# Kernel optimization log

Hardware: AMD Instinct MI355X
Metric: run time of the kernel (lower is better)

The kernel has to match this reference:

```python
import jax, jax.numpy as jnp
import numpy as np

B, N, IN_DIM, OUT_DIM, H = 4, 4096, 128, 128, 4
D = OUT_DIM // H  # head_dim = 32
NEG_SLOPE = 0.2


def setup_inputs() -> dict:
    key = jax.random.key(0)
    k_h, k_w = jax.random.split(key)
    h = jax.random.normal(k_h, (B, N, IN_DIM), dtype=jnp.float32)
    W = jax.random.normal(k_w, (OUT_DIM, IN_DIM), dtype=jnp.float32) * (1.0 / np.sqrt(IN_DIM))
    return {"h": h, "W": W}


def reference(h, W):
    b, n, _ = h.shape
    # Linear projection (no bias), split heads: [b, n, H, D]
    Wh = jnp.einsum('bni,oi->bno', h, W).reshape(b, n, H, D)
    # Per-head dense scores e = Wh @ Wh^T: [b, H, n, n]
    e = jnp.einsum('bnhd,bmhd->bhnm', Wh, Wh)
    # LeakyReLU-modified scores, row softmax (dropout = identity in eval)
    attn = jax.nn.softmax(jax.nn.leaky_relu(e, NEG_SLOPE), axis=-1)
    # Weighted aggregation: [b, n, H, D] -> [b, n, OUT_DIM]
    h_prime = jnp.einsum('bhnm,bmhd->bnhd', attn, Wh).reshape(b, n, H * D)
    return h_prime
```

## Files before the change

kernel.cpp:

```cpp
#include <hip/hip_runtime.h>

typedef __attribute__((ext_vector_type(8))) _Float16 f16x8;
typedef __attribute__((ext_vector_type(2))) __fp16 fp16x2;
typedef __attribute__((ext_vector_type(4))) float f32x4;
typedef __attribute__((ext_vector_type(4))) int i32x4;

#define NB 4
#define NN 4096
#define NH 4
#define ND 32
#define NEG_SL 0.2f
#define BQ 64
#define BK 128
#define KSTR 80
#define VSTR 272
#define CSC 1.2011224f
#define THR 10.0f

static __device__ __forceinline__ ushort f32_to_f16u(float f) {
  union { _Float16 h; ushort u; } c;
  c.h = (_Float16)f;
  return c.u;
}
static __device__ __forceinline__ float f16u_to_f32(ushort u) {
  union { _Float16 h; ushort u; } c;
  c.u = u;
  return (float)c.h;
}
static __device__ __forceinline__ unsigned cvt_pk_f16(float a, float b) {
  union { fp16x2 h; unsigned u; } c;
  c.h = __builtin_amdgcn_cvt_pkrtz(a, b);
  return c.u;
}
template <int CTRL>
static __device__ __forceinline__ float row_ror(float x) {
  return __int_as_float(__builtin_amdgcn_update_dpp(
      __float_as_int(x), __float_as_int(x), CTRL, 0xf, 0xf, true));
}
static __device__ __forceinline__ float rmax16(float v) {
  v = fmaxf(v, row_ror<0x121>(v));
  v = fmaxf(v, row_ror<0x122>(v));
  v = fmaxf(v, row_ror<0x124>(v));
  v = fmaxf(v, row_ror<0x128>(v));
  return v;
}
static __device__ __forceinline__ float rsum16(float v) {
  v += row_ror<0x121>(v);
  v += row_ror<0x122>(v);
  v += row_ror<0x124>(v);
  v += row_ror<0x128>(v);
  return v;
}

__global__ __launch_bounds__(256) void proj_kernel(const float* __restrict__ hm,
                                                   const float* __restrict__ Wm,
                                                   ushort* __restrict__ whh,
                                                   ushort* __restrict__ whl) {
  __shared__ float sWT[128 * 128];
  __shared__ float sH[64][128];

  const int t = threadIdx.x;
  const long rowbase = (long)blockIdx.x * 64;

  for (int i = t; i < 4096; i += 256) {
    const int o = i & 127, k4 = i >> 7;
    const float4 w = *(const float4*)(Wm + o * 128 + k4 * 4);
    sWT[(k4 * 4 + 0) * 128 + o] = w.x;
    sWT[(k4 * 4 + 1) * 128 + o] = w.y;
    sWT[(k4 * 4 + 2) * 128 + o] = w.z;
    sWT[(k4 * 4 + 3) * 128 + o] = w.w;
  }
  for (int i = t; i < 64 * 128 / 4; i += 256) {
    *((float4*)(&sH[0][0]) + i) = *((const float4*)(hm + rowbase * 128) + i);
  }
  __syncthreads();

  const int oc = (t & 31) * 4;
  const int nr = (t >> 5) * 8;

  float acc[8][4];
#pragma unroll
  for (int r = 0; r < 8; ++r)
#pragma unroll
    for (int j = 0; j < 4; ++j) acc[r][j] = 0.f;

  for (int k = 0; k < 128; ++k) {
    const float4 wv = *(const float4*)(&sWT[k * 128 + oc]);
#pragma unroll
    for (int r = 0; r < 8; ++r) {
      const float hv = sH[nr + r][k];
      acc[r][0] = fmaf(hv, wv.x, acc[r][0]);
      acc[r][1] = fmaf(hv, wv.y, acc[r][1]);
      acc[r][2] = fmaf(hv, wv.z, acc[r][2]);
      acc[r][3] = fmaf(hv, wv.w, acc[r][3]);
    }
  }

  const int hh = oc >> 5;
  const int d0 = oc & 31;
#pragma unroll
  for (int r = 0; r < 8; ++r) {
    const long gn = rowbase + nr + r;
    const long b = gn >> 12;
    const long n = gn & 4095;
    unsigned hi_[4], lo_[4];
#pragma unroll
    for (int j = 0; j < 4; ++j) {
      const float v = acc[r][j] * CSC;
      const ushort h16 = f32_to_f16u(v);
      hi_[j] = h16;
      lo_[j] = f32_to_f16u(v - f16u_to_f32(h16));
    }
    const size_t idx = (((size_t)(b * NH + hh)) * NN + n) * ND + d0;
    uint2 ph, pl;
    ph.x = hi_[0] | (hi_[1] << 16);
    ph.y = hi_[2] | (hi_[3] << 16);
    pl.x = lo_[0] | (lo_[1] << 16);
    pl.y = lo_[2] | (lo_[3] << 16);
    *(uint2*)(whh + idx) = ph;
    *(uint2*)(whl + idx) = pl;
  }
}

__global__ __launch_bounds__(256, 3) void attn_kernel(const ushort* __restrict__ whh,
                                                      const ushort* __restrict__ whl,
                                                      float* __restrict__ out) {
  __shared__ __align__(16) char sK[BK * KSTR];
  __shared__ __align__(16) char sVt[32 * VSTR];
  __shared__ __align__(16) char sP[4][6144];

  const int t = threadIdx.x;
  const int wid = t >> 6;
  const int lane = t & 63;
  const int qr = lane & 15;
  const int kg = lane >> 4;

  int bid = blockIdx.x;
  bid = (bid & 7) * 128 + (bid >> 3);
  const int qt = bid & 63;
  const int bh = bid >> 6;
  const ushort* __restrict__ baseh = whh + (size_t)bh * NN * ND;
  const ushort* __restrict__ basel = whl + (size_t)bh * NN * ND;

  const int q0 = qt * BQ + wid * 16;

  const f16x8 qh = *(const f16x8*)(baseh + (size_t)(q0 + qr) * ND + kg * 8);
  const f16x8 ql = *(const f16x8*)(basel + (size_t)(q0 + qr) * ND + kg * 8);

  const int kb = lane & 15;
  const int g = lane >> 4;
  const int s = wid;
  const int r0 = g * 32 + kb;
  const unsigned gsrc0 = (unsigned)(r0 * ND + s * 8);
  const unsigned gsrc1 = gsrc0 + 16u * ND;
  const unsigned kdst0 = (unsigned)(r0 * KSTR + ((s ^ (r0 & 3) ^ g) << 4));
  const unsigned kdst1 = kdst0 + 16u * KSTR;
  unsigned vaddr[8];
#pragma unroll
  for (int j = 0; j < 8; ++j) {
    const int d = s * 8 + j;
    const int B16 = (kb & 8) | ((kb + 3 * d + 2 * s) & 7);
    vaddr[j] = (unsigned)(d * VSTR + B16 * 16 + g * 4);
  }

  f32x4 o0 = {0.f, 0.f, 0.f, 0.f};
  f32x4 o1 = {0.f, 0.f, 0.f, 0.f};
  float m_[4], l_[4];
#pragma unroll
  for (int r = 0; r < 4; ++r) { m_[r] = -10000.f; l_[r] = 0.f; }

  i32x4 vh0 = *(const i32x4*)(baseh + gsrc0);
  i32x4 vh1 = *(const i32x4*)(baseh + gsrc1);

  for (int kt6 = 0; kt6 < 32; ++kt6) {
    __syncthreads();
    *(i32x4*)(&sK[kdst0]) = vh0;
    *(i32x4*)(&sK[kdst1]) = vh1;
#pragma unroll
    for (int j = 0; j < 8; ++j) {
      const int w = j >> 1;
      const unsigned a = (unsigned)vh0[w], b = (unsigned)vh1[w];
      const unsigned val = (j & 1) ? ((a >> 16) | (b & 0xffff0000u))
                                   : ((a & 0xffffu) | (b << 16));
      *(unsigned*)(&sVt[vaddr[j]]) = val;
    }
    const unsigned nb = (unsigned)(((kt6 + 1) & 31) * BK) * ND;
    vh0 = *(const i32x4*)(baseh + nb + gsrc0);
    vh1 = *(const i32x4*)(baseh + nb + gsrc1);
    __syncthreads();

    f32x4 acc[8];
#pragma unroll
    for (int ks = 0; ks < 8; ++ks) {
      const unsigned koff = (unsigned)((ks * 16 + qr) * KSTR) +
                            (unsigned)(((kg ^ (qr & 3) ^ (ks >> 1)) << 4));
      const f16x8 khf = *(const f16x8*)(&sK[koff]);
      f32x4 z = {0.f, 0.f, 0.f, 0.f};
      z = __builtin_amdgcn_mfma_f32_16x16x32_f16(ql, khf, z, 0, 0, 0);
      z = __builtin_amdgcn_mfma_f32_16x16x32_f16(qh, khf, z, 0, 0, 0);
      acc[ks] = z;
    }

    float pm[4];
#pragma unroll
    for (int r = 0; r < 4; ++r) pm[r] = -INFINITY;
#pragma unroll
    for (int ks = 0; ks < 8; ++ks)
#pragma unroll
      for (int r = 0; r < 4; ++r) {
        float x = acc[ks][r];
        x = fmaxf(x, NEG_SL * x);
        const float y = x - m_[r];
        acc[ks][r] = y;
        pm[r] = fmaxf(pm[r], y);
      }
    const float worst = fmaxf(fmaxf(pm[0], pm[1]), fmaxf(pm[2], pm[3]));
    if (__any(worst > THR)) {
#pragma unroll
      for (int r = 0; r < 4; ++r) {
        float d = rmax16(pm[r]);
        d = fmaxf(d, 0.f);
        m_[r] += d;
        const float sc = __builtin_amdgcn_exp2f(-d);
        l_[r] *= sc;
        o0[r] *= sc;
        o1[r] *= sc;
#pragma unroll
        for (int ks = 0; ks < 8; ++ks) acc[ks][r] -= d;
      }
    }

#pragma unroll
    for (int r = 0; r < 4; ++r) {
      i32x4 pw;
      float rs = 0.f;
#pragma unroll
      for (int w = 0; w < 4; ++w) {
        const float p0 = __builtin_amdgcn_exp2f(acc[2 * w][r]);
        const float p1 = __builtin_amdgcn_exp2f(acc[2 * w + 1][r]);
        rs += p0 + p1;
        pw[w] = (int)cvt_pk_f16(p0, p1);
      }
      l_[r] += rs;
      const int rho = kg * 4 + r;
      const int cb = qr ^ (rho & 7);
      *(i32x4*)(&sP[wid][rho * 256 + cb * 16]) = pw;
    }

#pragma unroll
    for (int kp = 0; kp < 4; ++kp) {
      const int kbR = kp * 4 + kg;
      const int cin = kbR + 3 * qr + 2 * (qr >> 3);
      const int cv0 = (kbR & 8) | (cin & 7);
      const int cv1 = (kbR & 8) | ((cin + 4) & 7);
      const f16x8 vb0 = *(const f16x8*)(&sVt[qr * VSTR + cv0 * 16]);
      const f16x8 vb1 = *(const f16x8*)(&sVt[(qr + 16) * VSTR + cv1 * 16]);
      const int cbp = kbR ^ (qr & 7);
      const f16x8 pa = *(const f16x8*)(&sP[wid][qr * 256 + cbp * 16]);
      o0 = __builtin_amdgcn_mfma_f32_16x16x32_f16(pa, vb0, o0, 0, 0, 0);
      o1 = __builtin_amdgcn_mfma_f32_16x16x32_f16(pa, vb1, o1, 0, 0, 0);
    }
  }

  const int b = bh >> 2, hh = bh & 3;
#pragma unroll
  for (int r = 0; r < 4; ++r) {
    const float lr = rsum16(l_[r]);
    const int q = q0 + kg * 4 + r;
    const float inv = 1.f / (CSC * lr);
    const size_t rowoff = ((size_t)(b * NN + q)) * 128 + hh * 32;
    out[rowoff + qr] = o0[r] * inv;
    out[rowoff + 16 + qr] = o1[r] * inv;
  }
}

extern "C" void kernel_launch(void* const* d_in, const int* in_sizes, int n_in,
                              void* d_out, int out_size, void* d_ws, size_t ws_size,
                              hipStream_t stream) {
  const float* hm = (const float*)d_in[0];
  const float* Wm = (const float*)d_in[1];
  float* out = (float*)d_out;
  ushort* whh = (ushort*)d_ws;
  ushort* whl = whh + (size_t)NB * NH * NN * ND;

  proj_kernel<<<NB * NN / 64, 256, 0, stream>>>(hm, Wm, whh, whl);
  attn_kernel<<<NB * NH * (NN / BQ), 256, 0, stream>>>(whh, whl, out);
}
```

Measured before the change: 126.9 us.

## Double query tile per block so each wave processes two 16-row query fragments

Raises the query tile from 64 to 128 rows, with each wave handling two 16-row fragments against the same K/V tile loaded into shared memory. This halves the K/V global loads and shared-memory staging per query, and reuses each K and V fragment read across two MFMA chains. In exchange it raises register pressure (launch bounds drop to 2 blocks per CU), grows the P buffer, and halves the grid to 512 blocks, which may underfill the GPU's compute units.

After: 119.3 us. -6.0%, faster.

```diff
diff --git a/kernel.cpp b/kernel.cpp
--- a/kernel.cpp
+++ b/kernel.cpp
@@ -10,7 +10,7 @@
 #define NH 4
 #define ND 32
 #define NEG_SL 0.2f
-#define BQ 64
+#define BQ 128
 #define BK 128
 #define KSTR 80
 #define VSTR 272
@@ -122,12 +122,12 @@
   }
 }
 
-__global__ __launch_bounds__(256, 3) void attn_kernel(const ushort* __restrict__ whh,
+__global__ __launch_bounds__(256, 2) void attn_kernel(const ushort* __restrict__ whh,
                                                       const ushort* __restrict__ whl,
                                                       float* __restrict__ out) {
   __shared__ __align__(16) char sK[BK * KSTR];
   __shared__ __align__(16) char sVt[32 * VSTR];
-  __shared__ __align__(16) char sP[4][6144];
+  __shared__ __align__(16) char sP[4][2][4096];
 
   const int t = threadIdx.x;
   const int wid = t >> 6;
@@ -136,16 +136,20 @@
   const int kg = lane >> 4;
 
   int bid = blockIdx.x;
-  bid = (bid & 7) * 128 + (bid >> 3);
-  const int qt = bid & 63;
-  const int bh = bid >> 6;
+  bid = (bid & 7) * 64 + (bid >> 3);
+  const int qt = bid & 31;
+  const int bh = bid >> 5;
   const ushort* __restrict__ baseh = whh + (size_t)bh * NN * ND;
   const ushort* __restrict__ basel = whl + (size_t)bh * NN * ND;
 
-  const int q0 = qt * BQ + wid * 16;
-
-  const f16x8 qh = *(const f16x8*)(baseh + (size_t)(q0 + qr) * ND + kg * 8);
-  const f16x8 ql = *(const f16x8*)(basel + (size_t)(q0 + qr) * ND + kg * 8);
+  const int q0 = qt * BQ + wid * 32;
+
+  f16x8 qh[2], ql[2];
+#pragma unroll
+  for (int qf = 0; qf < 2; ++qf) {
+    qh[qf] = *(const f16x8*)(baseh + (size_t)(q0 + qf * 16 + qr) * ND + kg * 8);
+    ql[qf] = *(const f16x8*)(basel + (size_t)(q0 + qf * 16 + qr) * ND + kg * 8);
+  }
 
   const int kb = lane & 15;
   const int g = lane >> 4;
@@ -163,11 +167,16 @@
     vaddr[j] = (unsigned)(d * VSTR + B16 * 16 + g * 4);
   }
 
-  f32x4 o0 = {0.f, 0.f, 0.f, 0.f};
-  f32x4 o1 = {0.f, 0.f, 0.f, 0.f};
-  float m_[4], l_[4];
-#pragma unroll
-  for (int r = 0; r < 4; ++r) { m_[r] = -10000.f; l_[r] = 0.f; }
+  f32x4 o[2][2];
+#pragma unroll
+  for (int qf = 0; qf < 2; ++qf)
+#pragma unroll
+    for (int pl = 0; pl < 2; ++pl) o[qf][pl] = f32x4{0.f, 0.f, 0.f, 0.f};
+  float m_[2][4], l_[2][4];
+#pragma unroll
+  for (int qf = 0; qf < 2; ++qf)
+#pragma unroll
+    for (int r = 0; r < 4; ++r) { m_[qf][r] = -10000.f; l_[qf][r] = 0.f; }
 
   i32x4 vh0 = *(const i32x4*)(baseh + gsrc0);
   i32x4 vh1 = *(const i32x4*)(baseh + gsrc1);
@@ -189,63 +198,78 @@
     vh1 = *(const i32x4*)(baseh + nb + gsrc1);
     __syncthreads();
 
-    f32x4 acc[8];
+    f32x4 acc[2][8];
 #pragma unroll
     for (int ks = 0; ks < 8; ++ks) {
       const unsigned koff = (unsigned)((ks * 16 + qr) * KSTR) +
                             (unsigned)(((kg ^ (qr & 3) ^ (ks >> 1)) << 4));
       const f16x8 khf = *(const f16x8*)(&sK[koff]);
-      f32x4 z = {0.f, 0.f, 0.f, 0.f};
-      z = __builtin_amdgcn_mfma_f32_16x16x32_f16(ql, khf, z, 0, 0, 0);
-      z = __builtin_amdgcn_mfma_f32_16x16x32_f16(qh, khf, z, 0, 0, 0);
-      acc[ks] = z;
-    }
-
-    float pm[4];
-#pragma unroll
-    for (int r = 0; r < 4; ++r) pm[r] = -INFINITY;
-#pragma unroll
-    for (int ks = 0; ks < 8; ++ks)
+#pragma unroll
+      for (int qf = 0; qf < 2; ++qf) {
+        f32x4 z = {0.f, 0.f, 0.f, 0.f};
+        z = __builtin_amdgcn_mfma_f32_16x16x32_f16(ql[qf], khf, z, 0, 0, 0);
+        z = __builtin_amdgcn_mfma_f32_16x16x32_f16(qh[qf], khf, z, 0, 0, 0);
+        acc[qf][ks] = z;
+      }
+    }
+
+    float pm[2][4];
+#pragma unroll
+    for (int qf = 0; qf < 2; ++qf)
+#pragma unroll
+      for (int r = 0; r < 4; ++r) pm[qf][r] = -INFINITY;
+#pragma unroll
+    for (int qf = 0; qf < 2; ++qf)
+#pragma unroll
+      for (int ks = 0; ks < 8; ++ks)
+#pragma unroll
+        for (int r = 0; r < 4; ++r) {
+          float x = acc[qf][ks][r];
+          x = fmaxf(x, NEG_SL * x);
+          const float y = x - m_[qf][r];
+          acc[qf][ks][r] = y;
+          pm[qf][r] = fmaxf(pm[qf][r], y);
+        }
+    float worst = -INFINITY;
+#pragma unroll
+    for (int qf = 0; qf < 2; ++qf)
+#pragma unroll
+      for (int r = 0; r < 4; ++r) worst = fmaxf(worst, pm[qf][r]);
+    if (__any(worst > THR)) {
+#pragma unroll
+      for (int qf = 0; qf < 2; ++qf)
+#pragma unroll
+        for (int r = 0; r < 4; ++r) {
+          float d = rmax16(pm[qf][r]);
+          d = fmaxf(d, 0.f);
+          m_[qf][r] += d;
+          const float sc = __builtin_amdgcn_exp2f(-d);
+          l_[qf][r] *= sc;
+          o[qf][0][r] *= sc;
+          o[qf][1][r] *= sc;
+#pragma unroll
+          for (int ks = 0; ks < 8; ++ks) acc[qf][ks][r] -= d;
+        }
+    }
+
+#pragma unroll
+    for (int qf = 0; qf < 2; ++qf)
 #pragma unroll
       for (int r = 0; r < 4; ++r) {
-        float x = acc[ks][r];
-        x = fmaxf(x, NEG_SL * x);
-        const float y = x - m_[r];
-        acc[ks][r] = y;
-        pm[r] = fmaxf(pm[r], y);
+        i32x4 pw;
+        float rs = 0.f;
+#pragma unroll
+        for (int w = 0; w < 4; ++w) {
+          const float p0 = __builtin_amdgcn_exp2f(acc[qf][2 * w][r]);
+          const float p1 = __builtin_amdgcn_exp2f(acc[qf][2 * w + 1][r]);
+          rs += p0 + p1;
+          pw[w] = (int)cvt_pk_f16(p0, p1);
+        }
+        l_[qf][r] += rs;
+        const int rho = kg * 4 + r;
+        const int cb = qr ^ (rho & 7);
+        *(i32x4*)(&sP[wid][qf][rho * 256 + cb * 16]) = pw;
       }
-    const float worst = fmaxf(fmaxf(pm[0], pm[1]), fmaxf(pm[2], pm[3]));
-    if (__any(worst > THR)) {
-#pragma unroll
-      for (int r = 0; r < 4; ++r) {
-        float d = rmax16(pm[r]);
-        d = fmaxf(d, 0.f);
-        m_[r] += d;
-        const float sc = __builtin_amdgcn_exp2f(-d);
-        l_[r] *= sc;
-        o0[r] *= sc;
-        o1[r] *= sc;
-#pragma unroll
-        for (int ks = 0; ks < 8; ++ks) acc[ks][r] -= d;
-      }
-    }
-
-#pragma unroll
-    for (int r = 0; r < 4; ++r) {
-      i32x4 pw;
-      float rs = 0.f;
-#pragma unroll
-      for (int w = 0; w < 4; ++w) {
-        const float p0 = __builtin_amdgcn_exp2f(acc[2 * w][r]);
-        const float p1 = __builtin_amdgcn_exp2f(acc[2 * w + 1][r]);
-        rs += p0 + p1;
-        pw[w] = (int)cvt_pk_f16(p0, p1);
-      }
-      l_[r] += rs;
-      const int rho = kg * 4 + r;
-      const int cb = qr ^ (rho & 7);
-      *(i32x4*)(&sP[wid][rho * 256 + cb * 16]) = pw;
-    }
 
 #pragma unroll
     for (int kp = 0; kp < 4; ++kp) {
@@ -256,22 +280,27 @@
       const f16x8 vb0 = *(const f16x8*)(&sVt[qr * VSTR + cv0 * 16]);
       const f16x8 vb1 = *(const f16x8*)(&sVt[(qr + 16) * VSTR + cv1 * 16]);
       const int cbp = kbR ^ (qr & 7);
-      const f16x8 pa = *(const f16x8*)(&sP[wid][qr * 256 + cbp * 16]);
-      o0 = __builtin_amdgcn_mfma_f32_16x16x32_f16(pa, vb0, o0, 0, 0, 0);
-      o1 = __builtin_amdgcn_mfma_f32_16x16x32_f16(pa, vb1, o1, 0, 0, 0);
+#pragma unroll
+      for (int qf = 0; qf < 2; ++qf) {
+        const f16x8 pa = *(const f16x8*)(&sP[wid][qf][qr * 256 + cbp * 16]);
+        o[qf][0] = __builtin_amdgcn_mfma_f32_16x16x32_f16(pa, vb0, o[qf][0], 0, 0, 0);
+        o[qf][1] = __builtin_amdgcn_mfma_f32_16x16x32_f16(pa, vb1, o[qf][1], 0, 0, 0);
+      }
     }
   }
 
   const int b = bh >> 2, hh = bh & 3;
 #pragma unroll
-  for (int r = 0; r < 4; ++r) {
-    const float lr = rsum16(l_[r]);
-    const int q = q0 + kg * 4 + r;
-    const float inv = 1.f / (CSC * lr);
-    const size_t rowoff = ((size_t)(b * NN + q)) * 128 + hh * 32;
-    out[rowoff + qr] = o0[r] * inv;
-    out[rowoff + 16 + qr] = o1[r] * inv;
-  }
+  for (int qf = 0; qf < 2; ++qf)
+#pragma unroll
+    for (int r = 0; r < 4; ++r) {
+      const float lr = rsum16(l_[qf][r]);
+      const int q = q0 + qf * 16 + kg * 4 + r;
+      const float inv = 1.f / (CSC * lr);
+      const size_t rowoff = ((size_t)(b * NN + q)) * 128 + hh * 32;
+      out[rowoff + qr] = o[qf][0][r] * inv;
+      out[rowoff + 16 + qr] = o[qf][1][r] * inv;
+    }
 }
 
 extern "C" void kernel_launch(void* const* d_in, const int* in_sizes, int n_in,
```
